# Kernel tuning notes

Hardware: AMD Instinct MI355X
Metric: run time of the kernel (lower is better)

## Reference

```python
import jax, jax.numpy as jnp
import numpy as np

HEADS = 4
DIM_HEAD = 32
SCALE = DIM_HEAD ** -0.5

# Energy conventions (Hopfield / Lagrangian formulation):
#  Neuron(x): g = activation(x); e = sum(x*g) - L(x)
#  Synapse(g, x): e = -sum(g*x)
#  identity Lagrangian: L(x) = 0.5*sum(x^2), g = x  => Conv2d block energy = -0.5*sum(x^2)
#  softmax Lagrangian: L(x) = sum(logsumexp(x, -1)), g = softmax(x, -1)

def setup_inputs() -> dict:
    key = jax.random.key(0)
    ks = jax.random.split(key, 5)
    b, c, h, w = 8, 256, 48, 48
    hidden = HEADS * DIM_HEAD  # 128
    return {
        "x": jax.random.normal(ks[0], (b, c, h, w), jnp.float32),
        "w_qkv": jax.random.normal(ks[1], (hidden * 3, c), jnp.float32) * 0.02,
        "b_qkv": jax.random.normal(ks[2], (hidden * 3,), jnp.float32) * 0.02,
        "w_out": jax.random.normal(ks[3], (c, hidden), jnp.float32) * 0.02,
        "b_out": jax.random.normal(ks[4], (c,), jnp.float32) * 0.02,
    }

def reference(x, w_qkv, b_qkv, w_out, b_out):
    b, c, h, w = x.shape
    # 1x1 conv == channel matmul
    qkv = jnp.einsum('oc,bcxy->boxy', w_qkv, x) + b_qkv[None, :, None, None]
    e_qkv = -0.5 * jnp.sum(qkv * qkv)  # identity-Lagrangian neuron + synapse energy
    q, k, v = jnp.split(qkv, 3, axis=1)
    # 'b (h c) x y -> b h c (x y)'
    def heads(t):
        return t.reshape(b, HEADS, DIM_HEAD, h * w)
    q, k, v = heads(q), heads(k), heads(v)
    q = q * SCALE
    sim = jnp.einsum('bhdi,bhdj->bhij', q, k)  # [b, heads, hw, hw]
    sim = sim - jax.lax.stop_gradient(jnp.max(sim, axis=-1, keepdims=True))
    attn = jax.nn.softmax(sim, axis=-1)
    # softmax-Lagrangian neuron energy: sum(sim*attn) - sum(logsumexp(sim, -1))
    e_attn = jnp.sum(sim * attn) - jnp.sum(jax.nn.logsumexp(sim, axis=-1))
    out = jnp.einsum('bhij,bhdj->bhid', attn, v)  # [b, heads, hw, dim_head]
    # 'b h (x y) d -> b (h d) x y'
    out = out.transpose(0, 1, 3, 2).reshape(b, HEADS * DIM_HEAD, h, w)
    out = jnp.einsum('oc,bcxy->boxy', w_out, out) + b_out[None, :, None, None]
    e_out = -0.5 * jnp.sum(out * out)
    return out, e_attn + e_out + e_qkv
```

## Files before the change

kernel.cpp:

```cpp
#include <hip/hip_runtime.h>
#include <hip/hip_bf16.h>

#define HW 2304
#define NB 8
#define NC 256
#define HID 128
#define DH 32
#define NH 4
#define SCALE 0.17677669529663687f
#define LOG2E 1.4426950408889634f
#define LN2   0.6931471805599453f

#define NSPLIT 4
#define OSZ ((size_t)NB * HW * HID)

using bf16x8 = __attribute__((ext_vector_type(8))) short;
using f32x4  = __attribute__((ext_vector_type(4))) float;

__device__ __forceinline__ short f2bf(float f) {
    unsigned u = __float_as_uint(f);
    u += 0x7FFF + ((u >> 16) & 1);
    return (short)(u >> 16);
}
__device__ __forceinline__ float bf2f(short s) {
    return __uint_as_float(((unsigned)(unsigned short)s) << 16);
}
__device__ __forceinline__ unsigned pk2bf(float a, float b) {
    union { __hip_bfloat162 h; unsigned u; } cv;
    cv.h = __float22bfloat162_rn(float2{a, b});
    return cv.u;
}
__device__ __forceinline__ void gld16(const void* g, void* l) {
    __builtin_amdgcn_global_load_lds(
        (const __attribute__((address_space(1))) unsigned*)g,
        (__attribute__((address_space(3))) unsigned*)l, 16, 0, 0);
}

__global__ __launch_bounds__(256)
void prep(const float* __restrict__ x, const float* __restrict__ wq,
          const float* __restrict__ wo, short* __restrict__ Xt,
          short* __restrict__ Wq, short* __restrict__ Wo, float* __restrict__ wsz)
{
    if (blockIdx.z == 8) {
        const int bid = blockIdx.x + 72 * blockIdx.y;
        if (bid == 0 && threadIdx.x == 0) { wsz[0] = 0.f; ((int*)wsz)[1] = 0; }
        const int i = bid * 256 + threadIdx.x;
        if (i < 384 * 256) Wq[i] = f2bf(wq[i]);
        if (i < 256 * 128) Wo[i] = f2bf(wo[i]);
        return;
    }
    __shared__ float T[32][33];
    const int b = blockIdx.z, c0 = blockIdx.y * 32, s0 = blockIdx.x * 32;
    const int ts = threadIdx.x & 31, tc = threadIdx.x >> 5;
    #pragma unroll
    for (int cc = tc; cc < 32; cc += 8)
        T[cc][ts] = x[((size_t)b * NC + c0 + cc) * HW + s0 + ts];
    __syncthreads();
    const int tcc = threadIdx.x & 31, tss = threadIdx.x >> 5;
    #pragma unroll
    for (int ss = tss; ss < 32; ss += 8)
        Xt[((size_t)b * HW + s0 + ss) * NC + c0 + tcc] = f2bf(T[tcc][ss]);
}

__global__ __launch_bounds__(256, 4)
void conv_qkv(const short* __restrict__ A, const short* __restrict__ Bt,
              const float* __restrict__ bias,
              short* __restrict__ Qb, short* __restrict__ Kb,
              short* __restrict__ Vb, float* __restrict__ E)
{
    constexpr int KD = NC;
    const int b  = blockIdx.z;
    const int bm = blockIdx.y * 64;
    const int bn = blockIdx.x * 128;
    const int t  = threadIdx.x;
    const int w  = t >> 6, lane = t & 63;
    const int n16 = lane & 15, quad = lane >> 4;

    __shared__ __align__(16) char csm[24576];
    __shared__ float red[4];

    const int rL = lane >> 2, cswz = (lane & 3) ^ (rL & 3);
    const char* agl = (const char*)(A  + (size_t)(bm + rL) * KD + cswz * 8);
    const char* bgl = (const char*)(Bt + ((size_t)b * HW + bn + rL) * KD + cswz * 8);

    auto issue = [&](int kc, int pbuf) {
        char* base = csm + pbuf * 12288;
        if (w == 0) {
            gld16(agl + (size_t)(0 * 16 * KD + kc) * 2, base + 0 * 1024);
            gld16(agl + (size_t)(1 * 16 * KD + kc) * 2, base + 1 * 1024);
            gld16(bgl + (size_t)(0 * 16 * KD + kc) * 2, base + 4096 + 0 * 1024);
        } else if (w == 1) {
            gld16(agl + (size_t)(2 * 16 * KD + kc) * 2, base + 2 * 1024);
            gld16(agl + (size_t)(3 * 16 * KD + kc) * 2, base + 3 * 1024);
            gld16(bgl + (size_t)(1 * 16 * KD + kc) * 2, base + 4096 + 1 * 1024);
        } else if (w == 2) {
            gld16(bgl + (size_t)(2 * 16 * KD + kc) * 2, base + 4096 + 2 * 1024);
            gld16(bgl + (size_t)(3 * 16 * KD + kc) * 2, base + 4096 + 3 * 1024);
            gld16(bgl + (size_t)(4 * 16 * KD + kc) * 2, base + 4096 + 4 * 1024);
        } else {
            gld16(bgl + (size_t)(5 * 16 * KD + kc) * 2, base + 4096 + 5 * 1024);
            gld16(bgl + (size_t)(6 * 16 * KD + kc) * 2, base + 4096 + 6 * 1024);
            gld16(bgl + (size_t)(7 * 16 * KD + kc) * 2, base + 4096 + 7 * 1024);
        }
    };

    f32x4 acc[4][2] = {};
    const int rsw = (quad ^ (n16 & 3)) * 16;
    constexpr int NI = KD / 32;

    issue(0, 0);
    for (int ki = 0; ki < NI; ++ki) {
        const int p = ki & 1;
        __syncthreads();
        if (ki + 1 < NI) issue((ki + 1) * 32, p ^ 1);

        const char* Ap = csm + p * 12288;
        const char* Bp = Ap + 4096;
        bf16x8 am[4], bq[2];
        #pragma unroll
        for (int tm = 0; tm < 4; ++tm)
            am[tm] = *(const bf16x8*)(Ap + tm * 1024 + n16 * 64 + rsw);
        #pragma unroll
        for (int j = 0; j < 2; ++j)
            bq[j] = *(const bf16x8*)(Bp + (w * 2 + j) * 1024 + n16 * 64 + rsw);
        #pragma unroll
        for (int tm = 0; tm < 4; ++tm)
            #pragma unroll
            for (int j = 0; j < 2; ++j)
                acc[tm][j] = __builtin_amdgcn_mfma_f32_16x16x32_bf16(am[tm], bq[j], acc[tm][j], 0, 0, 0);
    }

    float e = 0.f;
    #pragma unroll
    for (int tm = 0; tm < 4; ++tm) {
        const int o0 = bm + tm * 16 + quad * 4;
        const float4 bb = *(const float4*)(bias + o0);
        #pragma unroll
        for (int j = 0; j < 2; ++j) {
            const int s = bn + (w * 2 + j) * 16 + n16;
            float v[4] = {acc[tm][j][0] + bb.x, acc[tm][j][1] + bb.y,
                          acc[tm][j][2] + bb.z, acc[tm][j][3] + bb.w};
            e -= 0.5f * (v[0]*v[0] + v[1]*v[1] + v[2]*v[2] + v[3]*v[3]);
            if (o0 < HID) {
                const int h = o0 >> 5, dh0 = o0 & 31;
                const float qs = SCALE * LOG2E;
                short4 pk = {f2bf(v[0]*qs), f2bf(v[1]*qs),
                             f2bf(v[2]*qs), f2bf(v[3]*qs)};
                *(short4*)(Qb + ((size_t)(b * NH + h) * HW + s) * DH + dh0) = pk;
            } else if (o0 < 2 * HID) {
                const int c = o0 - HID, h = c >> 5, dh0 = c & 31;
                const int g = s & 31;
                const int sp = (s & ~31) | ((g & 4) << 2) | ((g >> 3) << 2) | (g & 3);
                short4 pk = {f2bf(v[0]), f2bf(v[1]), f2bf(v[2]), f2bf(v[3])};
                *(short4*)(Kb + ((size_t)(b * NH + h) * HW + sp) * DH + dh0) = pk;
            } else {
                const int c = o0 - 2 * HID, h = c >> 5, dh0 = c & 31;
                #pragma unroll
                for (int r = 0; r < 4; ++r)
                    Vb[((size_t)(b * NH + h) * DH + dh0 + r) * HW + s] = f2bf(v[r]);
            }
        }
    }

    #pragma unroll
    for (int off = 32; off > 0; off >>= 1) e += __shfl_down(e, off);
    if (lane == 0) red[w] = e;
    __syncthreads();
    if (t == 0) atomicAdd(E, red[0] + red[1] + red[2] + red[3]);
}

__global__ __launch_bounds__(256)
void flashsplit(const short* __restrict__ Qb, const short* __restrict__ Kb,
                const short* __restrict__ Vb, short* __restrict__ Oh,
                float* __restrict__ lsP, float* __restrict__ tsP)
{
    __shared__ __align__(16) char smem[16384];

    constexpr int ITERS = HW / (NSPLIT * 64);
    const int bh   = blockIdx.y;
    const int kh   = blockIdx.z;
    const int w    = threadIdx.x >> 6;
    const int lane = threadIdx.x & 63;
    const int n16  = lane & 15, quad = lane >> 4;
    const int qb   = blockIdx.x * 128 + w * 32;

    bf16x8 aq[2];
    #pragma unroll
    for (int qg = 0; qg < 2; ++qg)
        aq[qg] = *(const bf16x8*)(Qb + ((size_t)bh * HW + qb + qg * 16 + n16) * DH + quad * 8);

    const int rL = lane >> 2, cL = (lane & 3) ^ (rL & 3);
    const char* gbase; size_t gstep;
    if (w < 2) {
        gbase = (const char*)(Kb + (size_t)bh * HW * DH) + ((w & 1) * 16 + rL) * 64 + cL * 16;
        gstep = 2048;
    } else {
        gbase = (const char*)(Vb + (size_t)bh * DH * HW)
              + (size_t)((w & 1) * 16 + rL) * (HW * 2) + cL * 16;
        gstep = 64;
    }
    gbase += (size_t)kh * (2 * ITERS) * gstep;

    gld16(gbase,         smem + 0    + w * 1024);
    gld16(gbase + gstep, smem + 4096 + w * 1024);

    f32x4 acc[2][2] = {};
    float ls[2] = {}, ts[2] = {};
    const int swz = (quad ^ (n16 & 3)) * 8;

    for (int it = 0; it < ITERS; ++it) {
        const int p = it & 1;
        __syncthreads();
        if (it + 1 < ITERS) {
            const size_t g0 = (size_t)(2 * it + 2) * gstep;
            gld16(gbase + g0,         smem + (p ^ 1) * 8192 + 0    + w * 1024);
            gld16(gbase + g0 + gstep, smem + (p ^ 1) * 8192 + 4096 + w * 1024);
        }

        #pragma unroll
        for (int ca = 0; ca < 2; ++ca) {
            const short* kb = (const short*)(smem + p * 8192 + ca * 4096);

            const bf16x8 bk0 = *(const bf16x8*)(kb + n16 * 32 + swz);
            const bf16x8 bk1 = *(const bf16x8*)(kb + 512  + n16 * 32 + swz);
            const bf16x8 bv0 = *(const bf16x8*)(kb + 1024 + n16 * 32 + swz);
            const bf16x8 bv1 = *(const bf16x8*)(kb + 1536 + n16 * 32 + swz);

            #pragma unroll
            for (int qg = 0; qg < 2; ++qg) {
                f32x4 z = {};
                const f32x4 s0 = __builtin_amdgcn_mfma_f32_16x16x32_bf16(bk0, aq[qg], z, 0, 0, 0);
                const f32x4 s1 = __builtin_amdgcn_mfma_f32_16x16x32_bf16(bk1, aq[qg], z, 0, 0, 0);
                float e0[4], e1[4];
                #pragma unroll
                for (int r = 0; r < 4; ++r) {
                    e0[r] = __builtin_amdgcn_exp2f(s0[r]);
                    e1[r] = __builtin_amdgcn_exp2f(s1[r]);
                }
                ls[qg] += (e0[0] + e0[1]) + (e0[2] + e0[3])
                        + (e1[0] + e1[1]) + (e1[2] + e1[3]);
                ts[qg] += (e0[0]*s0[0] + e0[1]*s0[1]) + (e0[2]*s0[2] + e0[3]*s0[3])
                        + (e1[0]*s1[0] + e1[1]*s1[1]) + (e1[2]*s1[2] + e1[3]*s1[3]);
                union { bf16x8 v; unsigned u[4]; } pa;
                pa.u[0] = pk2bf(e0[0], e0[1]);
                pa.u[1] = pk2bf(e0[2], e0[3]);
                pa.u[2] = pk2bf(e1[0], e1[1]);
                pa.u[3] = pk2bf(e1[2], e1[3]);
                acc[qg][0] = __builtin_amdgcn_mfma_f32_16x16x32_bf16(bv0, pa.v, acc[qg][0], 0, 0, 0);
                acc[qg][1] = __builtin_amdgcn_mfma_f32_16x16x32_bf16(bv1, pa.v, acc[qg][1], 0, 0, 0);
            }
        }
    }

    #pragma unroll
    for (int qg = 0; qg < 2; ++qg) {
        ls[qg] += __shfl_xor(ls[qg], 16);
        ls[qg] += __shfl_xor(ls[qg], 32);
        ts[qg] += __shfl_xor(ts[qg], 16);
        ts[qg] += __shfl_xor(ts[qg], 32);
    }

    const int bb = bh >> 2, h = bh & 3;
    short* dst = Oh + (size_t)kh * OSZ;
    #pragma unroll
    for (int qg = 0; qg < 2; ++qg) {
        const int q = qb + qg * 16 + n16;
        const float L = ls[qg];
        const float invl = 1.f / L;
        short* ap = dst + ((size_t)bb * HW + q) * HID + h * 32;
        short4 pk0 = {f2bf(acc[qg][0][0] * invl), f2bf(acc[qg][0][1] * invl),
                      f2bf(acc[qg][0][2] * invl), f2bf(acc[qg][0][3] * invl)};
        short4 pk1 = {f2bf(acc[qg][1][0] * invl), f2bf(acc[qg][1][1] * invl),
                      f2bf(acc[qg][1][2] * invl), f2bf(acc[qg][1][3] * invl)};
        *(short4*)(ap + quad * 4)      = pk0;
        *(short4*)(ap + 16 + quad * 4) = pk1;
        if (quad == 0) {
            const size_t li = (size_t)(kh * 32 + bh) * HW + q;
            lsP[li] = L;
            tsP[li] = ts[qg];
        }
    }
}

__global__ __launch_bounds__(256, 2)
void conv_out(const short* __restrict__ A, const short* __restrict__ Oh,
              const float* __restrict__ lsP, const float* __restrict__ tsP,
              const float* __restrict__ bias, float* __restrict__ out0,
              float* __restrict__ E, int* __restrict__ ticket, int nblocks,
              float* __restrict__ edst)
{
    constexpr int KD = HID;
    constexpr int NI = KD / 32;
    const int b  = blockIdx.z;
    const int bm = blockIdx.y * 64;
    const int bn = blockIdx.x * 128;
    const int t  = threadIdx.x;
    const int w  = t >> 6, lane = t & 63;
    const int n16 = lane & 15, quad = lane >> 4;

    __shared__ __align__(16) char csm[24576];
    __shared__ float red[4];

    const int rL = lane >> 2, cswz = (lane & 3) ^ (rL & 3);
    const char* agl = (const char*)(A + (size_t)(bm + rL) * KD + cswz * 8);

    auto issueA = [&](int kc, int pbuf) {
        char* base = csm + pbuf * 12288;
        if (w == 0) {
            gld16(agl + (size_t)(0 * 16 * KD + kc) * 2, base + 0 * 1024);
            gld16(agl + (size_t)(1 * 16 * KD + kc) * 2, base + 1 * 1024);
        } else if (w == 1) {
            gld16(agl + (size_t)(2 * 16 * KD + kc) * 2, base + 2 * 1024);
            gld16(agl + (size_t)(3 * 16 * KD + kc) * 2, base + 3 * 1024);
        }
    };

    auto loadB = [&](int ki, bf16x8 pk[2]) {
        const int kc = ki * 32;
        const int bh = b * NH + ki;
        #pragma unroll
        for (int d = 0; d < 2; ++d) {
            const int blk = w * 2 + d;
            const int q = bn + blk * 16 + rL;
            float Ls[NSPLIT], sum = 0.f;
            #pragma unroll
            for (int kh = 0; kh < NSPLIT; ++kh) {
                Ls[kh] = lsP[(size_t)(kh * 32 + bh) * HW + q];
                sum += Ls[kh];
            }
            const float inv = 1.f / sum;
            float vv[8] = {};
            #pragma unroll
            for (int kh = 0; kh < NSPLIT; ++kh) {
                const float wk = Ls[kh] * inv;
                const bf16x8 o = *(const bf16x8*)(Oh + (size_t)kh * OSZ
                                    + ((size_t)b * HW + q) * HID + kc + cswz * 8);
                #pragma unroll
                for (int j = 0; j < 8; ++j) vv[j] += wk * bf2f(o[j]);
            }
            union { bf16x8 v; unsigned u[4]; } c;
            #pragma unroll
            for (int i = 0; i < 4; ++i) c.u[i] = pk2bf(vv[2*i], vv[2*i+1]);
            pk[d] = c.v;
        }
    };
    auto writeB = [&](const bf16x8 pk[2], int pbuf) {
        char* base = csm + pbuf * 12288 + 4096;
        #pragma unroll
        for (int d = 0; d < 2; ++d) {
            const int blk = w * 2 + d;
            *(bf16x8*)(base + blk * 1024 + rL * 64 + (lane & 3) * 16) = pk[d];
        }
    };

    f32x4 acc[4][2] = {};
    const int rsw = (quad ^ (n16 & 3)) * 16;

    bf16x8 bpk[2];
    loadB(0, bpk);
    issueA(0, 0);
    writeB(bpk, 0);
    for (int ki = 0; ki < NI; ++ki) {
        const int p = ki & 1;
        __syncthreads();
        if (ki + 1 < NI) { loadB(ki + 1, bpk); issueA((ki + 1) * 32, p ^ 1); }

        const char* Ap = csm + p * 12288;
        const char* Bp = Ap + 4096;
        bf16x8 am[4], bq[2];
        #pragma unroll
        for (int tm = 0; tm < 4; ++tm)
            am[tm] = *(const bf16x8*)(Ap + tm * 1024 + n16 * 64 + rsw);
        #pragma unroll
        for (int j = 0; j < 2; ++j)
            bq[j] = *(const bf16x8*)(Bp + (w * 2 + j) * 1024 + n16 * 64 + rsw);
        #pragma unroll
        for (int tm = 0; tm < 4; ++tm)
            #pragma unroll
            for (int j = 0; j < 2; ++j)
                acc[tm][j] = __builtin_amdgcn_mfma_f32_16x16x32_bf16(am[tm], bq[j], acc[tm][j], 0, 0, 0);

        if (ki + 1 < NI) writeB(bpk, p ^ 1);
    }

    float e = 0.f;
    #pragma unroll
    for (int tm = 0; tm < 4; ++tm) {
        const int o0 = bm + tm * 16 + quad * 4;
        const float4 bb = *(const float4*)(bias + o0);
        #pragma unroll
        for (int j = 0; j < 2; ++j) {
            const int s = bn + (w * 2 + j) * 16 + n16;
            float v[4] = {acc[tm][j][0] + bb.x, acc[tm][j][1] + bb.y,
                          acc[tm][j][2] + bb.z, acc[tm][j][3] + bb.w};
            e -= 0.5f * (v[0]*v[0] + v[1]*v[1] + v[2]*v[2] + v[3]*v[3]);
            #pragma unroll
            for (int r = 0; r < 4; ++r)
                out0[((size_t)b * NC + o0 + r) * HW + s] = v[r];
        }
    }

    if (blockIdx.y == 0) {
        const int q = bn + (t & 127);
        #pragma unroll
        for (int jj = 0; jj < 2; ++jj) {
            const int h = (t >> 7) * 2 + jj;
            const int bh = b * NH + h;
            float L = 0.f, T = 0.f;
            #pragma unroll
            for (int kh = 0; kh < NSPLIT; ++kh) {
                L += lsP[(size_t)(kh * 32 + bh) * HW + q];
                T += tsP[(size_t)(kh * 32 + bh) * HW + q];
            }
            e += (LN2 * T) / L - __logf(L);
        }
    }

    #pragma unroll
    for (int off = 32; off > 0; off >>= 1) e += __shfl_down(e, off);
    if (lane == 0) red[w] = e;
    __syncthreads();
    if (t == 0) {
        atomicAdd(E, red[0] + red[1] + red[2] + red[3]);
        __threadfence();
        const int prev = atomicAdd(ticket, 1);
        if (prev == nblocks - 1) {
            __threadfence();
            edst[0] = atomicAdd(E, 0.f);
        }
    }
}

extern "C" void kernel_launch(void* const* d_in, const int* in_sizes, int n_in,
                              void* d_out, int out_size, void* d_ws, size_t ws_size,
                              hipStream_t stream) {
    const float* x     = (const float*)d_in[0];
    const float* w_qkv = (const float*)d_in[1];
    const float* b_qkv = (const float*)d_in[2];
    const float* w_out = (const float*)d_in[3];
    const float* b_out = (const float*)d_in[4];
    float* out = (float*)d_out;

    float* wsf    = (float*)d_ws;
    float* E      = wsf;
    int*   ticket = (int*)d_ws + 1;
    short* Xt   = (short*)(wsf + 16);
    short* Wq   = Xt + (size_t)NB * HW * NC;
    short* Wo   = Wq + 384 * 256;
    short* Qb   = Wo + 256 * 128;
    short* Kb   = Qb + (size_t)NB * NH * HW * DH;
    short* Vb   = Kb + (size_t)NB * NH * HW * DH;
    short* Oh   = Vb + (size_t)NB * NH * HW * DH;
    float* lsP  = (float*)(Oh + NSPLIT * OSZ);
    float* tsP  = lsP + NSPLIT * 32 * HW;

    prep<<<dim3(HW / 32, NC / 32, NB + 1), 256, 0, stream>>>(
        x, w_qkv, w_out, Xt, Wq, Wo, wsf);
    conv_qkv<<<dim3(18, 6, NB), 256, 0, stream>>>(
        Wq, Xt, b_qkv, Qb, Kb, Vb, E);
    flashsplit<<<dim3(HW / 128, NB * NH, NSPLIT), 256, 0, stream>>>(
        Qb, Kb, Vb, Oh, lsP, tsP);
    conv_out<<<dim3(18, 4, NB), 256, 0, stream>>>(
        Wo, Oh, lsP, tsP, b_out, out, E, ticket, 18 * 4 * NB,
        out + (size_t)NB * NC * HW);
}
```

Measured before the change: 196.3 us.

## Deepen LDS prefetch to a 4-buffer ring with explicit vmcnt waits

Both conv_qkv and flashsplit move from a double-buffered LDS pipeline to a four-slot ring that keeps two tiles in flight. Each iteration waits with explicit s_waitcnt vmcnt counts plus a bare s_barrier, and sched_barrier stops the compiler from reordering around them. The aim is to hide global-load latency and remove the full __syncthreads drain on every iteration. In exchange, LDS use doubles, conv_qkv's launch bounds drop to 2 blocks per SM, occupancy may fall, and the hand-written vmcnt counts must exactly match the number of loads issued.

```diff
diff --git a/kernel.cpp b/kernel.cpp
--- a/kernel.cpp
+++ b/kernel.cpp
@@ -35,6 +35,7 @@
         (const __attribute__((address_space(1))) unsigned*)g,
         (__attribute__((address_space(3))) unsigned*)l, 16, 0, 0);
 }
+#define SB() __builtin_amdgcn_sched_barrier(0)
 
 __global__ __launch_bounds__(256)
 void prep(const float* __restrict__ x, const float* __restrict__ wq,
@@ -62,13 +63,14 @@
         Xt[((size_t)b * HW + s0 + ss) * NC + c0 + tcc] = f2bf(T[tcc][ss]);
 }
 
-__global__ __launch_bounds__(256, 4)
+__global__ __launch_bounds__(256, 2)
 void conv_qkv(const short* __restrict__ A, const short* __restrict__ Bt,
               const float* __restrict__ bias,
               short* __restrict__ Qb, short* __restrict__ Kb,
               short* __restrict__ Vb, float* __restrict__ E)
 {
     constexpr int KD = NC;
+    constexpr int NI = KD / 32;
     const int b  = blockIdx.z;
     const int bm = blockIdx.y * 64;
     const int bn = blockIdx.x * 128;
@@ -76,7 +78,7 @@
     const int w  = t >> 6, lane = t & 63;
     const int n16 = lane & 15, quad = lane >> 4;
 
-    __shared__ __align__(16) char csm[24576];
+    __shared__ __align__(16) char csm[4 * 12288];
     __shared__ float red[4];
 
     const int rL = lane >> 2, cswz = (lane & 3) ^ (rL & 3);
@@ -106,15 +108,22 @@
 
     f32x4 acc[4][2] = {};
     const int rsw = (quad ^ (n16 & 3)) * 16;
-    constexpr int NI = KD / 32;
-
-    issue(0, 0);
+
+    issue(0, 0); SB();
+    issue(32, 1); SB();
     for (int ki = 0; ki < NI; ++ki) {
-        const int p = ki & 1;
-        __syncthreads();
-        if (ki + 1 < NI) issue((ki + 1) * 32, p ^ 1);
-
-        const char* Ap = csm + p * 12288;
+        if (ki + 2 < NI) {
+            issue((ki + 2) * 32, (ki + 2) & 3);
+            asm volatile("s_waitcnt vmcnt(6)" ::: "memory");
+        } else if (ki + 2 == NI) {
+            asm volatile("s_waitcnt vmcnt(3)" ::: "memory");
+        } else {
+            asm volatile("s_waitcnt vmcnt(0)" ::: "memory");
+        }
+        __builtin_amdgcn_s_barrier();
+        SB();
+
+        const char* Ap = csm + (ki & 3) * 12288;
         const char* Bp = Ap + 4096;
         bf16x8 am[4], bq[2];
         #pragma unroll
@@ -174,7 +183,7 @@
                 const short* __restrict__ Vb, short* __restrict__ Oh,
                 float* __restrict__ lsP, float* __restrict__ tsP)
 {
-    __shared__ __align__(16) char smem[16384];
+    __shared__ __align__(16) char smem[4 * 8192];
 
     constexpr int ITERS = HW / (NSPLIT * 64);
     const int bh   = blockIdx.y;
@@ -188,6 +197,7 @@
     #pragma unroll
     for (int qg = 0; qg < 2; ++qg)
         aq[qg] = *(const bf16x8*)(Qb + ((size_t)bh * HW + qb + qg * 16 + n16) * DH + quad * 8);
+    SB();
 
     const int rL = lane >> 2, cL = (lane & 3) ^ (rL & 3);
     const char* gbase; size_t gstep;
@@ -201,25 +211,37 @@
     }
     gbase += (size_t)kh * (2 * ITERS) * gstep;
 
-    gld16(gbase,         smem + 0    + w * 1024);
-    gld16(gbase + gstep, smem + 4096 + w * 1024);
+    gld16(gbase,             smem + 0 * 8192 + 0    + w * 1024);
+    gld16(gbase + gstep,     smem + 0 * 8192 + 4096 + w * 1024);
+    SB();
+    gld16(gbase + 2 * gstep, smem + 1 * 8192 + 0    + w * 1024);
+    gld16(gbase + 3 * gstep, smem + 1 * 8192 + 4096 + w * 1024);
+    SB();
+    const char* gnext = gbase + 4 * gstep;
 
     f32x4 acc[2][2] = {};
     float ls[2] = {}, ts[2] = {};
     const int swz = (quad ^ (n16 & 3)) * 8;
 
     for (int it = 0; it < ITERS; ++it) {
-        const int p = it & 1;
-        __syncthreads();
-        if (it + 1 < ITERS) {
-            const size_t g0 = (size_t)(2 * it + 2) * gstep;
-            gld16(gbase + g0,         smem + (p ^ 1) * 8192 + 0    + w * 1024);
-            gld16(gbase + g0 + gstep, smem + (p ^ 1) * 8192 + 4096 + w * 1024);
-        }
-
+        if (it + 2 < ITERS) {
+            char* wb = smem + ((it + 2) & 3) * 8192;
+            gld16(gnext,         wb + 0    + w * 1024);
+            gld16(gnext + gstep, wb + 4096 + w * 1024);
+            gnext += 2 * gstep;
+            asm volatile("s_waitcnt vmcnt(4)" ::: "memory");
+        } else if (it + 2 == ITERS) {
+            asm volatile("s_waitcnt vmcnt(2)" ::: "memory");
+        } else {
+            asm volatile("s_waitcnt vmcnt(0)" ::: "memory");
+        }
+        __builtin_amdgcn_s_barrier();
+        SB();
+
+        const char* buf = smem + (it & 3) * 8192;
         #pragma unroll
         for (int ca = 0; ca < 2; ++ca) {
-            const short* kb = (const short*)(smem + p * 8192 + ca * 4096);
+            const short* kb = (const short*)(buf + ca * 4096);
 
             const bf16x8 bk0 = *(const bf16x8*)(kb + n16 * 32 + swz);
             const bf16x8 bk1 = *(const bf16x8*)(kb + 512  + n16 * 32 + swz);
```

New measurement: 197.1 us. Within noise of the previous version (+0.4%).
